# Kernel optimization log

Hardware: AMD Instinct MI355X
Metric: run time of the kernel (lower is better)

Reference implementation:

```python
import jax, jax.numpy as jnp
import numpy as np

NB_TF = 8
N_SEQ_TF = 2

# Concrete transform set (fixed magnitude 5 folded into constants), images in [0,1]

def _identity(v):
    return v

def _flip_lr(v):
    return v[..., ::-1]

def _flip_ud(v):
    return v[..., ::-1, :]

def _brightness(v):
    BRIGHT_FACTOR = 1.5  # mag 5 -> 1 + 5/10
    return jnp.clip(v * BRIGHT_FACTOR, 0.0, 1.0)

def _contrast(v):
    CONTRAST_FACTOR = 1.5
    mean = jnp.mean(v, axis=(-3, -2, -1), keepdims=True)  # per-image mean over C,H,W
    return jnp.clip((v - mean) * CONTRAST_FACTOR + mean, 0.0, 1.0)

def _solarize(v):
    THRESH = 0.5
    return jnp.where(v < THRESH, v, 1.0 - v)

def _invert(v):
    return 1.0 - v

def _posterize(v):
    LEVELS = 4.0  # mag 5 -> keep 2 bits
    return jnp.floor(v * LEVELS) / LEVELS

TFS = [_identity, _flip_lr, _flip_ud, _brightness, _contrast, _solarize, _invert, _posterize]


def setup_inputs() -> dict:
    key = jax.random.key(0)
    k1, k2, k3 = jax.random.split(key, 3)
    B, C, H, W = 128, 3, 224, 224
    x = jax.random.uniform(k1, (B, C, H, W), dtype=jnp.float32)
    prob = jax.random.uniform(k2, (NB_TF,), dtype=jnp.float32)  # learned routing param
    samples = jax.random.randint(k3, (N_SEQ_TF, B), 0, NB_TF, dtype=jnp.int32)
    return {"x": x, "prob": prob, "samples": samples}


def reference(x, prob, samples):
    # distrib is computed in the torch forward but only affects sampling (already
    # materialized in `samples`); recompute for faithfulness of the routing math.
    MIX = 0.5
    uniform = jax.nn.softmax(jnp.ones((NB_TF,), dtype=x.dtype))
    _distrib = jax.nn.softmax(MIX * prob + (1.0 - MIX) * uniform)  # noqa: F841

    out = x
    for step in range(samples.shape[0]):
        s = samples[step]  # [B] sampled TF index per image
        mask4 = s[:, None, None, None]  # broadcast over C,H,W
        y = jnp.zeros_like(out)
        # Equivalent of the boolean-mask gather/scatter dispatch: compute each
        # branch on the full batch and select per element (dense JAX analogue).
        for tf_idx, tf in enumerate(TFS):
            y = jnp.where(mask4 == tf_idx, tf(out), y)
        out = y
    return out
```

## Files before the change

### kernel.cpp

```cpp
#include <hip/hip_runtime.h>
#include <hip/hip_bf16.h>


#define B_    128
#define C_    3
#define H_    224
#define W_    224
#define N_ELEM (C_*H_*W_)
#define N4    (N_ELEM/4)
#define W4    (W_/4)
#define HW4   (H_*W4)
#define S_    8
#define CHUNK (N4/S_)
#define BPI   (N4/256)

__device__ __forceinline__ float apply_pw(float v, int tf, float mean) {
    switch (tf) {
        case 3: return fminf(fmaxf(v * 1.5f, 0.0f), 1.0f);
        case 4: return fminf(fmaxf((v - mean) * 1.5f + mean, 0.0f), 1.0f);
        case 5: return (v < 0.5f) ? v : (1.0f - v);
        case 6: return 1.0f - v;
        case 7: return floorf(v * 4.0f) * 0.25f;
        default: return v;
    }
}

__device__ __forceinline__ float block_reduce_sum(float v) {
    #pragma unroll
    for (int o = 32; o > 0; o >>= 1) v += __shfl_down(v, o, 64);
    __shared__ float smem[4];
    const int lane = threadIdx.x & 63, wid = threadIdx.x >> 6;
    if (lane == 0) smem[wid] = v;
    __syncthreads();
    return smem[0] + smem[1] + smem[2] + smem[3];
}

__global__ __launch_bounds__(256) void k_reduce0(const float* __restrict__ x,
                                                 const int* __restrict__ samples,
                                                 float* __restrict__ partial0) {
    const int img = blockIdx.x / S_, blk = blockIdx.x % S_;
    const int t0 = samples[img], t1 = samples[B_ + img];
    if (!(t0 == 4 || t1 == 4)) return;
    const float4* xi = (const float4*)x + (size_t)img * N4;
    const int start = blk * CHUNK, end = start + CHUNK;
    float acc = 0.0f;
    for (int i = start + threadIdx.x; i < end; i += 256) {
        float4 v = xi[i];
        acc += (v.x + v.y) + (v.z + v.w);
    }
    float tot = block_reduce_sum(acc);
    if (threadIdx.x == 0) partial0[img * S_ + blk] = tot;
}

__global__ __launch_bounds__(256) void k_reduce1(const float* __restrict__ x,
                                                 const int* __restrict__ samples,
                                                 const float* __restrict__ partial0,
                                                 float* __restrict__ partial1) {
    const int img = blockIdx.x / S_, blk = blockIdx.x % S_;
    const int t0 = samples[img], t1 = samples[B_ + img];
    if (!(t1 == 4 && t0 >= 3)) return;
    float mean0 = 0.0f;
    if (t0 == 4) {
        float s = 0.0f;
        #pragma unroll
        for (int i = 0; i < S_; ++i) s += partial0[img * S_ + i];
        mean0 = s * (1.0f / N_ELEM);
    }
    const float4* xi = (const float4*)x + (size_t)img * N4;
    const int start = blk * CHUNK, end = start + CHUNK;
    float acc = 0.0f;
    for (int i = start + threadIdx.x; i < end; i += 256) {
        float4 v = xi[i];
        acc += apply_pw(v.x, t0, mean0) + apply_pw(v.y, t0, mean0)
             + apply_pw(v.z, t0, mean0) + apply_pw(v.w, t0, mean0);
    }
    float tot = block_reduce_sum(acc);
    if (threadIdx.x == 0) partial1[img * S_ + blk] = tot;
}

__global__ __launch_bounds__(256) void k_apply(const float* __restrict__ x,
                                               const int* __restrict__ samples,
                                               const float* __restrict__ partial0,
                                               const float* __restrict__ partial1,
                                               float* __restrict__ out) {
    const int img = blockIdx.x / BPI;
    const int t0 = samples[img], t1 = samples[B_ + img];

    __shared__ float means[2];
    if (threadIdx.x == 0) {
        float m0 = 0.0f, m1 = 0.0f;
        if (t0 == 4 || t1 == 4) {
            float s = 0.0f;
            #pragma unroll
            for (int i = 0; i < S_; ++i) s += partial0[img * S_ + i];
            m0 = s * (1.0f / N_ELEM);
        }
        if (t1 == 4) {
            if (t0 < 3) m1 = m0;
            else {
                float s = 0.0f;
                #pragma unroll
                for (int i = 0; i < S_; ++i) s += partial1[img * S_ + i];
                m1 = s * (1.0f / N_ELEM);
            }
        }
        means[0] = m0; means[1] = m1;
    }
    __syncthreads();
    const float m0 = means[0], m1 = means[1];

    const bool fw = (t0 == 1) ^ (t1 == 1);
    const bool fh = (t0 == 2) ^ (t1 == 2);

    const int tid = (blockIdx.x % BPI) * 256 + threadIdx.x;
    const int c = tid / HW4, rem = tid % HW4;
    const int h = rem / W4, wq = rem % W4;
    const int hs  = fh ? (H_ - 1 - h)  : h;
    const int wqs = fw ? (W4 - 1 - wq) : wq;

    const float4* xi = (const float4*)x + (size_t)img * N4;
    float4 v = xi[c * HW4 + hs * W4 + wqs];
    if (fw) { float t = v.x; v.x = v.w; v.w = t; t = v.y; v.y = v.z; v.z = t; }

    v.x = apply_pw(apply_pw(v.x, t0, m0), t1, m1);
    v.y = apply_pw(apply_pw(v.y, t0, m0), t1, m1);
    v.z = apply_pw(apply_pw(v.z, t0, m0), t1, m1);
    v.w = apply_pw(apply_pw(v.w, t0, m0), t1, m1);

    ((float4*)out)[(size_t)img * N4 + tid] = v;
}

extern "C" void kernel_launch(void* const* d_in, const int* in_sizes, int n_in,
                              void* d_out, int out_size, void* d_ws, size_t ws_size,
                              hipStream_t stream) {
    const float* x       = (const float*)d_in[0];
    const int*   samples = (const int*)d_in[2];
    float*       out     = (float*)d_out;

    float* partial0 = (float*)d_ws;
    float* partial1 = partial0 + B_ * S_;

    k_reduce0<<<B_ * S_, 256, 0, stream>>>(x, samples, partial0);
    k_reduce1<<<B_ * S_, 256, 0, stream>>>(x, samples, partial0, partial1);
    k_apply  <<<B_ * BPI, 256, 0, stream>>>(x, samples, partial0, partial1, out);
}
```

Baseline: 156.9 us.

## Fuse reduce and apply into one cooperative kernel with grid syncs

Replaces the three launches (two mean reductions and the apply pass) with a single cooperative kernel of 1024 blocks that synchronizes the grid twice. The second-step mean is computed in the same pass as the first where it does not depend on the first mean (brightness, solarize, posterize), and is derived in closed form for invert. Only the contrast-after-contrast case needs an extra pass. Each block now handles one eighth of an image in the apply phase, so the chunk it just reduced may still be in cache. In exchange it pays the cost of grid-wide barriers and a cooperative launch, and it relies on all blocks being resident at once.

```diff
diff --git a/kernel.cpp b/kernel.cpp
--- a/kernel.cpp
+++ b/kernel.cpp
@@ -1,5 +1,8 @@
 #include <hip/hip_runtime.h>
 #include <hip/hip_bf16.h>
+#include <hip/hip_cooperative_groups.h>
+
+namespace cg = cooperative_groups;
 
 
 #define B_    128
@@ -12,7 +15,6 @@
 #define HW4   (H_*W4)
 #define S_    8
 #define CHUNK (N4/S_)
-#define BPI   (N4/256)
 
 __device__ __forceinline__ float apply_pw(float v, int tf, float mean) {
     switch (tf) {
@@ -25,80 +27,85 @@
     }
 }
 
-__device__ __forceinline__ float block_reduce_sum(float v) {
+__device__ __forceinline__ float2 block_reduce_sum2(float a, float b) {
     #pragma unroll
-    for (int o = 32; o > 0; o >>= 1) v += __shfl_down(v, o, 64);
-    __shared__ float smem[4];
+    for (int o = 32; o > 0; o >>= 1) {
+        a += __shfl_down(a, o, 64);
+        b += __shfl_down(b, o, 64);
+    }
+    __shared__ float2 smem[4];
     const int lane = threadIdx.x & 63, wid = threadIdx.x >> 6;
-    if (lane == 0) smem[wid] = v;
     __syncthreads();
-    return smem[0] + smem[1] + smem[2] + smem[3];
+    if (lane == 0) smem[wid] = make_float2(a, b);
+    __syncthreads();
+    float2 r;
+    r.x = ((smem[0].x + smem[1].x) + (smem[2].x + smem[3].x));
+    r.y = ((smem[0].y + smem[1].y) + (smem[2].y + smem[3].y));
+    return r;
 }
 
-__global__ __launch_bounds__(256) void k_reduce0(const float* __restrict__ x,
-                                                 const int* __restrict__ samples,
-                                                 float* __restrict__ partial0) {
-    const int img = blockIdx.x / S_, blk = blockIdx.x % S_;
+__global__ __launch_bounds__(256, 4) void k_fused(const float* __restrict__ x,
+                                                  const int* __restrict__ samples,
+                                                  float* __restrict__ ws,
+                                                  float* __restrict__ out) {
+    cg::grid_group gg = cg::this_grid();
+    const int img = blockIdx.x >> 3, blk = blockIdx.x & 7;
     const int t0 = samples[img], t1 = samples[B_ + img];
-    if (!(t0 == 4 || t1 == 4)) return;
+    float* partial0 = ws;
+    float* partial1 = ws + B_ * S_;
     const float4* xi = (const float4*)x + (size_t)img * N4;
-    const int start = blk * CHUNK, end = start + CHUNK;
-    float acc = 0.0f;
-    for (int i = start + threadIdx.x; i < end; i += 256) {
-        float4 v = xi[i];
-        acc += (v.x + v.y) + (v.z + v.w);
+
+    const bool need0  = (t0 == 4) || (t1 == 4);
+    const bool need1e = (t1 == 4) && (t0 == 3 || t0 == 5 || t0 == 7);
+
+    if (need0) {
+        float a0 = 0.f, a1 = 0.f;
+        for (int i = threadIdx.x; i < CHUNK; i += 256) {
+            float4 v = xi[blk * CHUNK + i];
+            a0 += (v.x + v.y) + (v.z + v.w);
+            if (need1e) {
+                a1 += apply_pw(v.x, t0, 0.f) + apply_pw(v.y, t0, 0.f)
+                    + apply_pw(v.z, t0, 0.f) + apply_pw(v.w, t0, 0.f);
+            }
+        }
+        float2 r = block_reduce_sum2(a0, a1);
+        if (threadIdx.x == 0) {
+            partial0[img * S_ + blk] = r.x;
+            if (need1e) partial1[img * S_ + blk] = r.y;
+        }
     }
-    float tot = block_reduce_sum(acc);
-    if (threadIdx.x == 0) partial0[img * S_ + blk] = tot;
-}
+    gg.sync();
 
-__global__ __launch_bounds__(256) void k_reduce1(const float* __restrict__ x,
-                                                 const int* __restrict__ samples,
-                                                 const float* __restrict__ partial0,
-                                                 float* __restrict__ partial1) {
-    const int img = blockIdx.x / S_, blk = blockIdx.x % S_;
-    const int t0 = samples[img], t1 = samples[B_ + img];
-    if (!(t1 == 4 && t0 >= 3)) return;
-    float mean0 = 0.0f;
-    if (t0 == 4) {
-        float s = 0.0f;
+    if (t0 == 4 && t1 == 4) {
+        float s = 0.f;
         #pragma unroll
         for (int i = 0; i < S_; ++i) s += partial0[img * S_ + i];
-        mean0 = s * (1.0f / N_ELEM);
+        const float m0c = s * (1.0f / N_ELEM);
+        float a1 = 0.f;
+        for (int i = threadIdx.x; i < CHUNK; i += 256) {
+            float4 v = xi[blk * CHUNK + i];
+            a1 += apply_pw(v.x, 4, m0c) + apply_pw(v.y, 4, m0c)
+                + apply_pw(v.z, 4, m0c) + apply_pw(v.w, 4, m0c);
+        }
+        float2 r = block_reduce_sum2(a1, 0.f);
+        if (threadIdx.x == 0) partial1[img * S_ + blk] = r.x;
     }
-    const float4* xi = (const float4*)x + (size_t)img * N4;
-    const int start = blk * CHUNK, end = start + CHUNK;
-    float acc = 0.0f;
-    for (int i = start + threadIdx.x; i < end; i += 256) {
-        float4 v = xi[i];
-        acc += apply_pw(v.x, t0, mean0) + apply_pw(v.y, t0, mean0)
-             + apply_pw(v.z, t0, mean0) + apply_pw(v.w, t0, mean0);
-    }
-    float tot = block_reduce_sum(acc);
-    if (threadIdx.x == 0) partial1[img * S_ + blk] = tot;
-}
-
-__global__ __launch_bounds__(256) void k_apply(const float* __restrict__ x,
-                                               const int* __restrict__ samples,
-                                               const float* __restrict__ partial0,
-                                               const float* __restrict__ partial1,
-                                               float* __restrict__ out) {
-    const int img = blockIdx.x / BPI;
-    const int t0 = samples[img], t1 = samples[B_ + img];
+    gg.sync();
 
     __shared__ float means[2];
     if (threadIdx.x == 0) {
-        float m0 = 0.0f, m1 = 0.0f;
-        if (t0 == 4 || t1 == 4) {
-            float s = 0.0f;
+        float m0 = 0.f, m1 = 0.f;
+        if (need0) {
+            float s = 0.f;
             #pragma unroll
             for (int i = 0; i < S_; ++i) s += partial0[img * S_ + i];
             m0 = s * (1.0f / N_ELEM);
         }
         if (t1 == 4) {
-            if (t0 < 3) m1 = m0;
+            if (t0 < 3)       m1 = m0;
+            else if (t0 == 6) m1 = 1.0f - m0;
             else {
-                float s = 0.0f;
+                float s = 0.f;
                 #pragma unroll
                 for (int i = 0; i < S_; ++i) s += partial1[img * S_ + i];
                 m1 = s * (1.0f / N_ELEM);
@@ -112,22 +119,21 @@
     const bool fw = (t0 == 1) ^ (t1 == 1);
     const bool fh = (t0 == 2) ^ (t1 == 2);
 
-    const int tid = (blockIdx.x % BPI) * 256 + threadIdx.x;
-    const int c = tid / HW4, rem = tid % HW4;
-    const int h = rem / W4, wq = rem % W4;
-    const int hs  = fh ? (H_ - 1 - h)  : h;
-    const int wqs = fw ? (W4 - 1 - wq) : wq;
-
-    const float4* xi = (const float4*)x + (size_t)img * N4;
-    float4 v = xi[c * HW4 + hs * W4 + wqs];
-    if (fw) { float t = v.x; v.x = v.w; v.w = t; t = v.y; v.y = v.z; v.z = t; }
-
-    v.x = apply_pw(apply_pw(v.x, t0, m0), t1, m1);
-    v.y = apply_pw(apply_pw(v.y, t0, m0), t1, m1);
-    v.z = apply_pw(apply_pw(v.z, t0, m0), t1, m1);
-    v.w = apply_pw(apply_pw(v.w, t0, m0), t1, m1);
-
-    ((float4*)out)[(size_t)img * N4 + tid] = v;
+    float4* oi = (float4*)out + (size_t)img * N4;
+    for (int i = threadIdx.x; i < CHUNK; i += 256) {
+        const int idx = blk * CHUNK + i;
+        const int c = idx / HW4, rem = idx % HW4;
+        const int h = rem / W4, wq = rem % W4;
+        const int hs  = fh ? (H_ - 1 - h)  : h;
+        const int wqs = fw ? (W4 - 1 - wq) : wq;
+        float4 v = xi[c * HW4 + hs * W4 + wqs];
+        if (fw) { float t = v.x; v.x = v.w; v.w = t; t = v.y; v.y = v.z; v.z = t; }
+        v.x = apply_pw(apply_pw(v.x, t0, m0), t1, m1);
+        v.y = apply_pw(apply_pw(v.y, t0, m0), t1, m1);
+        v.z = apply_pw(apply_pw(v.z, t0, m0), t1, m1);
+        v.w = apply_pw(apply_pw(v.w, t0, m0), t1, m1);
+        oi[idx] = v;
+    }
 }
 
 extern "C" void kernel_launch(void* const* d_in, const int* in_sizes, int n_in,
@@ -136,11 +142,9 @@
     const float* x       = (const float*)d_in[0];
     const int*   samples = (const int*)d_in[2];
     float*       out     = (float*)d_out;
+    float*       ws      = (float*)d_ws;
 
-    float* partial0 = (float*)d_ws;
-    float* partial1 = partial0 + B_ * S_;
-
-    k_reduce0<<<B_ * S_, 256, 0, stream>>>(x, samples, partial0);
-    k_reduce1<<<B_ * S_, 256, 0, stream>>>(x, samples, partial0, partial1);
-    k_apply  <<<B_ * BPI, 256, 0, stream>>>(x, samples, partial0, partial1, out);
+    void* args[] = { (void*)&x, (void*)&samples, (void*)&ws, (void*)&out };
+    hipLaunchCooperativeKernel((const void*)k_fused, dim3(B_ * S_), dim3(256),
+                               args, 0, stream);
 }
```

Measured after the change: 395.9 us. +152.3%, slower.
